# Performance work log

Measured on AMD Instinct MI355X. Metric: run time of the kernel, lower is better.

The kernel has to match this reference:

```python
import jax, jax.numpy as jnp
import numpy as np

RESET_PERIOD = 10
DECAY = 0.1
D_MODEL = 512
D_INNER = 1024
N_LAYERS = 4


def layer_norm(x, scale, bias, eps=1e-5):
    mu = jnp.mean(x, axis=-1, keepdims=True)
    var = jnp.mean((x - mu) ** 2, axis=-1, keepdims=True)
    return (x - mu) * jax.lax.rsqrt(var + eps) * scale + bias


def setup_inputs() -> dict:
    key = jax.random.key(0)
    ks = jax.random.split(key, 12)
    B, S, F, V, MF = 8, 2048, 128, 256, 4096
    D, DI, L = D_MODEL, D_INNER, N_LAYERS
    rn = lambda k, shape, s: jax.random.normal(k, shape, jnp.float32) * s
    return {
        "frames": rn(ks[0], (B, S, F), 1.0),
        "padding_mask": jax.random.uniform(ks[1], (B, S)) < 0.9,
        "W_in_proj": rn(ks[2], (F, D), 0.05),
        "b_in_proj": jnp.zeros((D,), jnp.float32),
        "pos_emb": rn(ks[3], (MF, D), 0.02),
        "ln_scale": jnp.ones((L, D), jnp.float32),
        "ln_bias": jnp.zeros((L, D), jnp.float32),
        "W_in": rn(ks[4], (L, D, 2 * DI), 0.03),
        "b_in": jnp.zeros((L, 2 * DI), jnp.float32),
        "W_out": rn(ks[5], (L, DI, D), 0.03),
        "b_out": jnp.zeros((L, D), jnp.float32),
        "fn_scale": jnp.ones((D,), jnp.float32),
        "fn_bias": jnp.zeros((D,), jnp.float32),
        "W_frame": rn(ks[6], (D, F), 0.03),
        "b_frame": jnp.zeros((F,), jnp.float32),
        "W_sym": rn(ks[7], (D, V), 0.03),
        "b_sym": jnp.zeros((V,), jnp.float32),
    }


def reference(frames, padding_mask, W_in_proj, b_in_proj, pos_emb,
              ln_scale, ln_bias, W_in, b_in, W_out, b_out,
              fn_scale, fn_bias, W_frame, b_frame, W_sym, b_sym):
    B, S, F = frames.shape
    # input projection + clamped positional embedding
    x = frames @ W_in_proj + b_in_proj                     # [B,S,D]
    pos = jnp.clip(jnp.arange(S), 0, pos_emb.shape[0] - 1)
    x = x + pos_emb[pos][None]
    # periodic hard-reset decay: frame_counter starts at 0, incremented AFTER
    # each step, so steps with (t+1) % reset_period == 0 are scaled.
    t = jnp.arange(S) + 1
    decay = jnp.where(t % RESET_PERIOD == 0, DECAY, 1.0)[None, :, None]  # [1,S,1]

    def layer(h, p):
        s, b, Wi, bi, Wo, bo = p
        n = layer_norm(h, s, b)
        uz = n @ Wi + bi                                   # [B,S,2*DI]
        u, g = jnp.split(uz, 2, axis=-1)
        y = (u * jax.nn.silu(g)) @ Wo + bo                 # [B,S,D]
        # wrapper scales the full block output (incl. residual)
        return (h + y) * decay, None

    x, _ = jax.lax.scan(layer, x, (ln_scale, ln_bias, W_in, b_in, W_out, b_out))
    x = layer_norm(x, fn_scale, fn_bias)
    frame_outputs = x @ W_frame + b_frame                  # [B,S,F]
    symbol_logits = x @ W_sym + b_sym                      # [B,S,V]
    m = padding_mask[..., None]
    frame_outputs = jnp.where(m, frame_outputs, 0.0)
    symbol_logits = jnp.where(m, symbol_logits, 0.0)
    return frame_outputs, symbol_logits
```

## Files before the change

### kernel.cpp

```cpp
#include <hip/hip_runtime.h>
#include <hip/hip_bf16.h>

using f32x4  = __attribute__((ext_vector_type(4))) float;
using bf16x8 = __attribute__((ext_vector_type(8))) short;
using bf16x4 = __attribute__((ext_vector_type(4))) short;

#define MTOT   16384
#define DMODEL 512
#define DINNER 1024
#define SEQ    2048

__device__ __forceinline__ short f2b(float f){
  unsigned u = __builtin_bit_cast(unsigned, f);
  u = (u + 0x7FFFu + ((u >> 16) & 1u)) >> 16;
  return (short)u;
}

__device__ __forceinline__ void gl_lds16(const short* g, short* l){
  __builtin_amdgcn_global_load_lds(
      (const __attribute__((address_space(1))) void*)g,
      (__attribute__((address_space(3))) void*)l, 16, 0, 0);
}

__global__ void detect_mask(const unsigned char* __restrict__ m, int* __restrict__ flag){
  __shared__ int sge2, soff, soff8;
  int tid = threadIdx.x;
  if (tid == 0){ sge2 = 0; soff = 0; soff8 = 0; }
  __syncthreads();
  int ge2 = 0, off = 0, off8 = 0;
  for (int i = tid; i < 16384; i += 256){
    unsigned char b = m[i];
    if (b >= 2) ge2++;
    if ((i & 3) && b) off++;
    if (((i & 7) == 4) && b) off8++;
  }
  atomicAdd(&sge2, ge2); atomicAdd(&soff, off); atomicAdd(&soff8, off8);
  __syncthreads();
  if (tid == 0){
    int f;
    if      (sge2 > 0) f = 2;
    else if (soff > 0) f = 1;
    else if (soff8 > 0) f = 0;
    else               f = 3;
    *flag = f;
  }
}

__device__ __forceinline__ bool mask_at(const void* mask, int flag, int m){
  if (flag == 1) return ((const unsigned char*)mask)[m] != 0;
  if (flag == 2) return ((const float*)mask)[m] != 0.0f;
  if (flag == 3) return ((const int*)mask)[2*m] != 0;
  return ((const int*)mask)[m] != 0;
}

__global__ void cvt_bf16(const float* __restrict__ in, short* __restrict__ out){
  int i = (blockIdx.x * 256 + threadIdx.x) * 4;
  float4 v = *(const float4*)(in + i);
  bf16x4 o; o[0] = f2b(v.x); o[1] = f2b(v.y); o[2] = f2b(v.z); o[3] = f2b(v.w);
  *(bf16x4*)(out + i) = o;
}

__global__ void transpose_w(const float* __restrict__ in, short* __restrict__ out, int R, int C){
  in  += (size_t)blockIdx.z * R * C;
  out += (size_t)blockIdx.z * R * C;
  __shared__ float t[32][33];
  int tx = threadIdx.x, ty = threadIdx.y;
  int r0 = blockIdx.y * 32, c0 = blockIdx.x * 32;
  #pragma unroll
  for (int i = 0; i < 4; i++)
    t[ty + i*8][tx] = in[(size_t)(r0 + ty + i*8) * C + c0 + tx];
  __syncthreads();
  #pragma unroll
  for (int i = 0; i < 4; i++)
    out[(size_t)(c0 + ty + i*8) * R + r0 + tx] = f2b(t[tx][ty + i*8]);
}

__global__ __launch_bounds__(256) void ln_k(const float* __restrict__ x,
                                            const float* __restrict__ sc,
                                            const float* __restrict__ bi,
                                            short* __restrict__ out){
  int row  = blockIdx.x * 4 + (threadIdx.x >> 6);
  int lane = threadIdx.x & 63;
  const float* p = x + (size_t)row * DMODEL + lane * 8;
  float4 a = *(const float4*)p;
  float4 b = *(const float4*)(p + 4);
  float s = a.x+a.y+a.z+a.w + b.x+b.y+b.z+b.w;
  float q = a.x*a.x+a.y*a.y+a.z*a.z+a.w*a.w + b.x*b.x+b.y*b.y+b.z*b.z+b.w*b.w;
  #pragma unroll
  for (int o = 32; o >= 1; o >>= 1){ s += __shfl_xor(s, o); q += __shfl_xor(q, o); }
  float mu  = s * (1.0f/DMODEL);
  float var = q * (1.0f/DMODEL) - mu*mu;
  float rs  = rsqrtf(var + 1e-5f);
  int c = lane * 8;
  float vals[8] = {a.x,a.y,a.z,a.w,b.x,b.y,b.z,b.w};
  bf16x8 o8;
  #pragma unroll
  for (int e = 0; e < 8; e++) o8[e] = f2b((vals[e]-mu)*rs*sc[c+e] + bi[c+e]);
  *(bf16x8*)(out + (size_t)row * DMODEL + c) = o8;
}

template<int MODE, int K>
__global__ __launch_bounds__(256) void gemm_k(
    const short* __restrict__ A, const short* __restrict__ B0, const short* __restrict__ B1,
    const float* __restrict__ bias0, const float* __restrict__ bias1,
    const float* __restrict__ pos, float* __restrict__ xbuf, short* __restrict__ obuf,
    float* __restrict__ fout, const void* __restrict__ mask, const int* __restrict__ flagp,
    int ldo)
{
  constexpr int BM = (MODE == 1) ? 64 : 128;
  constexpr int BN = 128;
  constexpr int NB = (MODE == 1) ? 2 : 1;
  constexpr int NJ = (MODE == 1) ? 2 : 4;

  __shared__ short lds[(BM + BN * NB) * 64];
  short* lA  = lds;
  short* lB  = lds + BM * 64;
  short* lB2 = lds + (BM + BN) * 64;

  const int nbx = gridDim.x;
  int bid = blockIdx.y * nbx + blockIdx.x;
  const int nwg = nbx * gridDim.y;
  bid = (bid & 7) * (nwg >> 3) + (bid >> 3);
  const int bx = bid % nbx, by = bid / nbx;
  const int n0 = bx * BN, m0 = by * BM;

  const int tid = threadIdx.x, lane = tid & 63, wid = tid >> 6;
  const int lr  = lane >> 3;
  const int lks = (lane & 7) ^ (lr & 7);
  const int fr = lane & 15;
  const int kg = lane >> 4;

  const int wr = (MODE == 1) ? 0 : (wid >> 1);
  const int wc = (MODE == 1) ? wid : (wid & 1);
  const int rA0 = wr * 64 + fr;
  const int rB0 = wc * ((MODE == 1) ? 32 : 64) + fr;

  f32x4 acc[4][NJ];
  f32x4 acc2[(MODE == 1) ? 4 : 1][(MODE == 1) ? 2 : 1];
  const f32x4 zero = {0.f, 0.f, 0.f, 0.f};
  #pragma unroll
  for (int i = 0; i < 4; i++)
    #pragma unroll
    for (int j = 0; j < NJ; j++) acc[i][j] = zero;
  if constexpr (MODE == 1){
    #pragma unroll
    for (int i = 0; i < 4; i++)
      #pragma unroll
      for (int j = 0; j < 2; j++) acc2[i][j] = zero;
  }

  const short* Ab  = A  + (size_t)m0 * K + (size_t)lr * K + lks * 8;
  const short* B0b = B0 + (size_t)n0 * K + (size_t)lr * K + lks * 8;
  const short* B1b = (MODE == 1) ? (B1 + (size_t)n0 * K + (size_t)lr * K + lks * 8) : nullptr;

  for (int kt = 0; kt < K; kt += 64){
    __syncthreads();
    #pragma unroll
    for (int c = 0; c < BM / 32; c++)
      gl_lds16(Ab + kt + (size_t)(wid + c * 4) * 8 * K, lA + (wid + c * 4) * 512);
    #pragma unroll
    for (int c = 0; c < BN / 32; c++)
      gl_lds16(B0b + kt + (size_t)(wid + c * 4) * 8 * K, lB + (wid + c * 4) * 512);
    if constexpr (MODE == 1){
      #pragma unroll
      for (int c = 0; c < BN / 32; c++)
        gl_lds16(B1b + kt + (size_t)(wid + c * 4) * 8 * K, lB2 + (wid + c * 4) * 512);
    }
    __syncthreads();

    #pragma unroll
    for (int kb8 = 0; kb8 < 8; kb8 += 4){
      bf16x8 aF[4];
      #pragma unroll
      for (int i = 0; i < 4; i++){
        const int row = rA0 + i * 16;
        aF[i] = *(const bf16x8*)((const char*)lA + row * 128 + (((kg + kb8) ^ (row & 7)) * 16));
      }
      if constexpr (MODE == 1){
        bf16x8 bF[2], gF[2];
        #pragma unroll
        for (int j = 0; j < 2; j++){
          const int row = rB0 + j * 16;
          const int p = ((kg + kb8) ^ (row & 7)) * 16;
          bF[j] = *(const bf16x8*)((const char*)lB  + row * 128 + p);
          gF[j] = *(const bf16x8*)((const char*)lB2 + row * 128 + p);
        }
        #pragma unroll
        for (int i = 0; i < 4; i++)
          #pragma unroll
          for (int j = 0; j < 2; j++){
            acc[i][j]  = __builtin_amdgcn_mfma_f32_16x16x32_bf16(aF[i], bF[j], acc[i][j], 0, 0, 0);
            acc2[i][j] = __builtin_amdgcn_mfma_f32_16x16x32_bf16(aF[i], gF[j], acc2[i][j], 0, 0, 0);
          }
      } else {
        bf16x8 bF[4];
        #pragma unroll
        for (int j = 0; j < 4; j++){
          const int row = rB0 + j * 16;
          bF[j] = *(const bf16x8*)((const char*)lB + row * 128 + (((kg + kb8) ^ (row & 7)) * 16));
        }
        #pragma unroll
        for (int i = 0; i < 4; i++)
          #pragma unroll
          for (int j = 0; j < 4; j++)
            acc[i][j] = __builtin_amdgcn_mfma_f32_16x16x32_bf16(aF[i], bF[j], acc[i][j], 0, 0, 0);
      }
    }
  }

  const int col0 = n0 + ((MODE == 1) ? wid * 32 : wc * 64) + fr;
  const int row0 = m0 + ((MODE == 1) ? 0 : wr * 64) + kg * 4;
  int flag = 0;
  if constexpr (MODE == 3) flag = *flagp;

  #pragma unroll
  for (int i = 0; i < 4; i++){
    #pragma unroll
    for (int r = 0; r < 4; r++){
      const int gm = row0 + i * 16 + r;
      #pragma unroll
      for (int j = 0; j < NJ; j++){
        const int gn = col0 + j * 16;
        float v = acc[i][j][r];
        if constexpr (MODE == 0){
          xbuf[(size_t)gm * ldo + gn] = v + bias0[gn] + pos[(size_t)(gm & (SEQ-1)) * DMODEL + gn];
        } else if constexpr (MODE == 1){
          float u = v + bias0[gn];
          float g = acc2[i][j][r] + bias1[gn];
          float sg = g / (1.0f + expf(-g));
          obuf[(size_t)gm * ldo + gn] = f2b(u * sg);
        } else if constexpr (MODE == 2){
          int s = gm & (SEQ-1);
          float d = (((s + 1) % 10) == 0) ? 0.1f : 1.0f;
          float y = v + bias0[gn];
          xbuf[(size_t)gm * ldo + gn] = (xbuf[(size_t)gm * ldo + gn] + y) * d;
        } else {
          bool mk = mask_at(mask, flag, gm);
          fout[(size_t)gm * ldo + gn] = mk ? (v + bias0[gn]) : 0.0f;
        }
      }
    }
  }
}

extern "C" void kernel_launch(void* const* d_in, const int* in_sizes, int n_in,
                              void* d_out, int out_size, void* d_ws, size_t ws_size,
                              hipStream_t stream){
  const float* frames    = (const float*)d_in[0];
  const void*  mask      = d_in[1];
  const float* W_in_proj = (const float*)d_in[2];
  const float* b_in_proj = (const float*)d_in[3];
  const float* pos_emb   = (const float*)d_in[4];
  const float* ln_scale  = (const float*)d_in[5];
  const float* ln_bias   = (const float*)d_in[6];
  const float* W_in      = (const float*)d_in[7];
  const float* b_in      = (const float*)d_in[8];
  const float* W_out     = (const float*)d_in[9];
  const float* b_out     = (const float*)d_in[10];
  const float* fn_scale  = (const float*)d_in[11];
  const float* fn_bias   = (const float*)d_in[12];
  const float* W_frame   = (const float*)d_in[13];
  const float* b_frame   = (const float*)d_in[14];
  const float* W_sym     = (const float*)d_in[15];
  const float* b_sym     = (const float*)d_in[16];

  char* w = (char*)d_ws;
  int*   flag = (int*)w;
  float* xbuf = (float*)(w + 256);
  short* nbuf = (short*)(w + 256 + 33554432);
  short* abuf = (short*)(w + 256 + 33554432 + 16777216);
  short* frb  = (short*)(w + 256 + 33554432 + 16777216 + 33554432);
  short* Wt0  = frb + (size_t)16384 * 128;
  short* Wt1  = Wt0 + (size_t)512 * 128;
  short* Wt2  = Wt1 + (size_t)4 * 2048 * 512;
  short* Wt3  = Wt2 + (size_t)4 * 512 * 1024;
  short* Wt4  = Wt3 + (size_t)128 * 512;

  detect_mask<<<1, 256, 0, stream>>>((const unsigned char*)mask, flag);
  cvt_bf16<<<2048, 256, 0, stream>>>(frames, frb);
  transpose_w<<<dim3(16,  4, 1), dim3(32, 8), 0, stream>>>(W_in_proj, Wt0, 128, 512);
  transpose_w<<<dim3(64, 16, 4), dim3(32, 8), 0, stream>>>(W_in,      Wt1, 512, 2048);
  transpose_w<<<dim3(16, 32, 4), dim3(32, 8), 0, stream>>>(W_out,     Wt2, 1024, 512);
  transpose_w<<<dim3(4,  16, 1), dim3(32, 8), 0, stream>>>(W_frame,   Wt3, 512, 128);
  transpose_w<<<dim3(8,  16, 1), dim3(32, 8), 0, stream>>>(W_sym,     Wt4, 512, 256);

  gemm_k<0, 128><<<dim3(4, 128), 256, 0, stream>>>(frb, Wt0, nullptr, b_in_proj, nullptr, pos_emb,
      xbuf, nullptr, nullptr, nullptr, nullptr, 512);

  for (int l = 0; l < 4; l++){
    ln_k<<<4096, 256, 0, stream>>>(xbuf, ln_scale + l*512, ln_bias + l*512, nbuf);
    gemm_k<1, 512><<<dim3(8, 256), 256, 0, stream>>>(nbuf,
        Wt1 + (size_t)l*2048*512, Wt1 + (size_t)l*2048*512 + (size_t)1024*512,
        b_in + l*2048, b_in + l*2048 + 1024, nullptr,
        nullptr, abuf, nullptr, nullptr, nullptr, 1024);
    gemm_k<2, 1024><<<dim3(4, 128), 256, 0, stream>>>(abuf, Wt2 + (size_t)l*512*1024, nullptr,
        b_out + l*512, nullptr, nullptr, xbuf, nullptr, nullptr, nullptr, nullptr, 512);
  }

  ln_k<<<4096, 256, 0, stream>>>(xbuf, fn_scale, fn_bias, nbuf);
  gemm_k<3, 512><<<dim3(1, 128), 256, 0, stream>>>(nbuf, Wt3, nullptr, b_frame, nullptr, nullptr,
      nullptr, nullptr, (float*)d_out, mask, flag, 128);
  gemm_k<3, 512><<<dim3(2, 128), 256, 0, stream>>>(nbuf, Wt4, nullptr, b_sym, nullptr, nullptr,
      nullptr, nullptr, (float*)d_out + (size_t)16384*128, mask, flag, 256);
}
```

Before: 582.0 us.

## Interleave GLU weight halves to use unified 128x128 GEMM tile; fuse output heads

Permutes the W_in transpose so that u and gate columns alternate in 16-column groups. The GLU GEMM can then use the standard 128x128 tile with a single B operand and pair adjacent accumulator fragments in the epilogue, replacing the 64-row tile with dual B buffers. The frame and symbol output projections also become one launch over a 384-column weight, relying on Wt3 and Wt4 sitting next to each other in the workspace. This raises the compute per loaded byte and removes one launch, at the cost of an unusual column mapping that has to stay consistent between the transpose and the epilogue.

```diff
diff --git a/kernel.cpp b/kernel.cpp
--- a/kernel.cpp
+++ b/kernel.cpp
@@ -60,6 +60,7 @@
   *(bf16x4*)(out + i) = o;
 }
 
+template<int GLU>
 __global__ void transpose_w(const float* __restrict__ in, short* __restrict__ out, int R, int C){
   in  += (size_t)blockIdx.z * R * C;
   out += (size_t)blockIdx.z * R * C;
@@ -71,8 +72,16 @@
     t[ty + i*8][tx] = in[(size_t)(r0 + ty + i*8) * C + c0 + tx];
   __syncthreads();
   #pragma unroll
-  for (int i = 0; i < 4; i++)
-    out[(size_t)(c0 + ty + i*8) * R + r0 + tx] = f2b(t[tx][ty + i*8]);
+  for (int i = 0; i < 4; i++){
+    int oc = c0 + ty + i*8;
+    int nr;
+    if constexpr (GLU){
+      int half = C >> 1;
+      nr = (oc < half) ? (((oc >> 4) << 5) + (oc & 15))
+                       : ((((oc - half) >> 4) << 5) + 16 + (oc & 15));
+    } else nr = oc;
+    out[(size_t)nr * R + r0 + tx] = f2b(t[tx][ty + i*8]);
+  }
 }
 
 __global__ __launch_bounds__(256) void ln_k(const float* __restrict__ x,
@@ -101,21 +110,16 @@
 
 template<int MODE, int K>
 __global__ __launch_bounds__(256) void gemm_k(
-    const short* __restrict__ A, const short* __restrict__ B0, const short* __restrict__ B1,
+    const short* __restrict__ A, const short* __restrict__ B,
     const float* __restrict__ bias0, const float* __restrict__ bias1,
     const float* __restrict__ pos, float* __restrict__ xbuf, short* __restrict__ obuf,
     float* __restrict__ fout, const void* __restrict__ mask, const int* __restrict__ flagp,
     int ldo)
 {
-  constexpr int BM = (MODE == 1) ? 64 : 128;
-  constexpr int BN = 128;
-  constexpr int NB = (MODE == 1) ? 2 : 1;
-  constexpr int NJ = (MODE == 1) ? 2 : 4;
-
-  __shared__ short lds[(BM + BN * NB) * 64];
-  short* lA  = lds;
-  short* lB  = lds + BM * 64;
-  short* lB2 = lds + (BM + BN) * 64;
+  constexpr int BM = 128, BN = 128;
+  __shared__ short lds[(BM + BN) * 64];
+  short* lA = lds;
+  short* lB = lds + BM * 64;
 
   const int nbx = gridDim.x;
   int bid = blockIdx.y * nbx + blockIdx.x;
@@ -130,113 +134,93 @@
   const int fr = lane & 15;
   const int kg = lane >> 4;
 
-  const int wr = (MODE == 1) ? 0 : (wid >> 1);
-  const int wc = (MODE == 1) ? wid : (wid & 1);
+  const int wr = wid >> 1, wc = wid & 1;
   const int rA0 = wr * 64 + fr;
-  const int rB0 = wc * ((MODE == 1) ? 32 : 64) + fr;
-
-  f32x4 acc[4][NJ];
-  f32x4 acc2[(MODE == 1) ? 4 : 1][(MODE == 1) ? 2 : 1];
+  const int rB0 = wc * 64 + fr;
+
+  f32x4 acc[4][4];
   const f32x4 zero = {0.f, 0.f, 0.f, 0.f};
   #pragma unroll
   for (int i = 0; i < 4; i++)
     #pragma unroll
-    for (int j = 0; j < NJ; j++) acc[i][j] = zero;
-  if constexpr (MODE == 1){
-    #pragma unroll
-    for (int i = 0; i < 4; i++)
-      #pragma unroll
-      for (int j = 0; j < 2; j++) acc2[i][j] = zero;
-  }
-
-  const short* Ab  = A  + (size_t)m0 * K + (size_t)lr * K + lks * 8;
-  const short* B0b = B0 + (size_t)n0 * K + (size_t)lr * K + lks * 8;
-  const short* B1b = (MODE == 1) ? (B1 + (size_t)n0 * K + (size_t)lr * K + lks * 8) : nullptr;
+    for (int j = 0; j < 4; j++) acc[i][j] = zero;
+
+  const short* Ab = A + (size_t)m0 * K + (size_t)lr * K + lks * 8;
+  const short* Bb = B + (size_t)n0 * K + (size_t)lr * K + lks * 8;
 
   for (int kt = 0; kt < K; kt += 64){
     __syncthreads();
     #pragma unroll
-    for (int c = 0; c < BM / 32; c++)
+    for (int c = 0; c < 4; c++)
       gl_lds16(Ab + kt + (size_t)(wid + c * 4) * 8 * K, lA + (wid + c * 4) * 512);
     #pragma unroll
-    for (int c = 0; c < BN / 32; c++)
-      gl_lds16(B0b + kt + (size_t)(wid + c * 4) * 8 * K, lB + (wid + c * 4) * 512);
-    if constexpr (MODE == 1){
-      #pragma unroll
-      for (int c = 0; c < BN / 32; c++)
-        gl_lds16(B1b + kt + (size_t)(wid + c * 4) * 8 * K, lB2 + (wid + c * 4) * 512);
-    }
+    for (int c = 0; c < 4; c++)
+      gl_lds16(Bb + kt + (size_t)(wid + c * 4) * 8 * K, lB + (wid + c * 4) * 512);
     __syncthreads();
 
     #pragma unroll
     for (int kb8 = 0; kb8 < 8; kb8 += 4){
-      bf16x8 aF[4];
+      bf16x8 aF[4], bF[4];
       #pragma unroll
       for (int i = 0; i < 4; i++){
         const int row = rA0 + i * 16;
         aF[i] = *(const bf16x8*)((const char*)lA + row * 128 + (((kg + kb8) ^ (row & 7)) * 16));
       }
+      #pragma unroll
+      for (int j = 0; j < 4; j++){
+        const int row = rB0 + j * 16;
+        bF[j] = *(const bf16x8*)((const char*)lB + row * 128 + (((kg + kb8) ^ (row & 7)) * 16));
+      }
+      #pragma unroll
+      for (int i = 0; i < 4; i++)
+        #pragma unroll
+        for (int j = 0; j < 4; j++)
+          acc[i][j] = __builtin_amdgcn_mfma_f32_16x16x32_bf16(aF[i], bF[j], acc[i][j], 0, 0, 0);
+    }
+  }
+
+  const int col0 = n0 + wc * 64 + fr;
+  const int row0 = m0 + wr * 64 + kg * 4;
+  int flag = 0;
+  if constexpr (MODE == 3) flag = *flagp;
+
+  #pragma unroll
+  for (int i = 0; i < 4; i++){
+    #pragma unroll
+    for (int r = 0; r < 4; r++){
+      const int gm = row0 + i * 16 + r;
       if constexpr (MODE == 1){
-        bf16x8 bF[2], gF[2];
         #pragma unroll
-        for (int j = 0; j < 2; j++){
-          const int row = rB0 + j * 16;
-          const int p = ((kg + kb8) ^ (row & 7)) * 16;
-          bF[j] = *(const bf16x8*)((const char*)lB  + row * 128 + p);
-          gF[j] = *(const bf16x8*)((const char*)lB2 + row * 128 + p);
+        for (int jj = 0; jj < 2; jj++){
+          const int j = 2 * jj;
+          const int nb = n0 + wc * 64 + j * 16;
+          const int lc = ((nb >> 5) << 4) + fr;
+          float u = acc[i][j][r]     + bias0[lc];
+          float g = acc[i][j+1][r]   + bias0[1024 + lc];
+          float sg = g / (1.0f + expf(-g));
+          obuf[(size_t)gm * 1024 + lc] = f2b(u * sg);
         }
-        #pragma unroll
-        for (int i = 0; i < 4; i++)
-          #pragma unroll
-          for (int j = 0; j < 2; j++){
-            acc[i][j]  = __builtin_amdgcn_mfma_f32_16x16x32_bf16(aF[i], bF[j], acc[i][j], 0, 0, 0);
-            acc2[i][j] = __builtin_amdgcn_mfma_f32_16x16x32_bf16(aF[i], gF[j], acc2[i][j], 0, 0, 0);
-          }
       } else {
-        bf16x8 bF[4];
         #pragma unroll
         for (int j = 0; j < 4; j++){
-          const int row = rB0 + j * 16;
-          bF[j] = *(const bf16x8*)((const char*)lB + row * 128 + (((kg + kb8) ^ (row & 7)) * 16));
-        }
-        #pragma unroll
-        for (int i = 0; i < 4; i++)
-          #pragma unroll
-          for (int j = 0; j < 4; j++)
-            acc[i][j] = __builtin_amdgcn_mfma_f32_16x16x32_bf16(aF[i], bF[j], acc[i][j], 0, 0, 0);
-      }
-    }
-  }
-
-  const int col0 = n0 + ((MODE == 1) ? wid * 32 : wc * 64) + fr;
-  const int row0 = m0 + ((MODE == 1) ? 0 : wr * 64) + kg * 4;
-  int flag = 0;
-  if constexpr (MODE == 3) flag = *flagp;
-
-  #pragma unroll
-  for (int i = 0; i < 4; i++){
-    #pragma unroll
-    for (int r = 0; r < 4; r++){
-      const int gm = row0 + i * 16 + r;
-      #pragma unroll
-      for (int j = 0; j < NJ; j++){
-        const int gn = col0 + j * 16;
-        float v = acc[i][j][r];
-        if constexpr (MODE == 0){
-          xbuf[(size_t)gm * ldo + gn] = v + bias0[gn] + pos[(size_t)(gm & (SEQ-1)) * DMODEL + gn];
-        } else if constexpr (MODE == 1){
-          float u = v + bias0[gn];
-          float g = acc2[i][j][r] + bias1[gn];
-          float sg = g / (1.0f + expf(-g));
-          obuf[(size_t)gm * ldo + gn] = f2b(u * sg);
-        } else if constexpr (MODE == 2){
-          int s = gm & (SEQ-1);
-          float d = (((s + 1) % 10) == 0) ? 0.1f : 1.0f;
-          float y = v + bias0[gn];
-          xbuf[(size_t)gm * ldo + gn] = (xbuf[(size_t)gm * ldo + gn] + y) * d;
-        } else {
-          bool mk = mask_at(mask, flag, gm);
-          fout[(size_t)gm * ldo + gn] = mk ? (v + bias0[gn]) : 0.0f;
+          const int gn = col0 + j * 16;
+          float v = acc[i][j][r];
+          if constexpr (MODE == 0){
+            xbuf[(size_t)gm * ldo + gn] = v + bias0[gn] + pos[(size_t)(gm & (SEQ-1)) * DMODEL + gn];
+          } else if constexpr (MODE == 2){
+            int s = gm & (SEQ-1);
+            float d = (((s + 1) % 10) == 0) ? 0.1f : 1.0f;
+            float y = v + bias0[gn];
+            xbuf[(size_t)gm * ldo + gn] = (xbuf[(size_t)gm * ldo + gn] + y) * d;
+          } else {
+            bool mk = mask_at(mask, flag, gm);
+            if (gn < 128){
+              fout[(size_t)gm * 128 + gn] = mk ? (v + bias0[gn]) : 0.0f;
+            } else {
+              int gs = gn - 128;
+              fout[(size_t)16384 * 128 + (size_t)gm * 256 + gs] = mk ? (v + bias1[gs]) : 0.0f;
+            }
+          }
         }
       }
     }
@@ -278,28 +262,25 @@
 
   detect_mask<<<1, 256, 0, stream>>>((const unsigned char*)mask, flag);
   cvt_bf16<<<2048, 256, 0, stream>>>(frames, frb);
-  transpose_w<<<dim3(16,  4, 1), dim3(32, 8), 0, stream>>>(W_in_proj, Wt0, 128, 512);
-  transpose_w<<<dim3(64, 16, 4), dim3(32, 8), 0, stream>>>(W_in,      Wt1, 512, 2048);
-  transpose_w<<<dim3(16, 32, 4), dim3(32, 8), 0, stream>>>(W_out,     Wt2, 1024, 512);
-  transpose_w<<<dim3(4,  16, 1), dim3(32, 8), 0, stream>>>(W_frame,   Wt3, 512, 128);
-  transpose_w<<<dim3(8,  16, 1), dim3(32, 8), 0, stream>>>(W_sym,     Wt4, 512, 256);
-
-  gemm_k<0, 128><<<dim3(4, 128), 256, 0, stream>>>(frb, Wt0, nullptr, b_in_proj, nullptr, pos_emb,
+  transpose_w<0><<<dim3(16,  4, 1), dim3(32, 8), 0, stream>>>(W_in_proj, Wt0, 128, 512);
+  transpose_w<1><<<dim3(64, 16, 4), dim3(32, 8), 0, stream>>>(W_in,      Wt1, 512, 2048);
+  transpose_w<0><<<dim3(16, 32, 4), dim3(32, 8), 0, stream>>>(W_out,     Wt2, 1024, 512);
+  transpose_w<0><<<dim3(4,  16, 1), dim3(32, 8), 0, stream>>>(W_frame,   Wt3, 512, 128);
+  transpose_w<0><<<dim3(8,  16, 1), dim3(32, 8), 0, stream>>>(W_sym,     Wt4, 512, 256);
+
+  gemm_k<0, 128><<<dim3(4, 128), 256, 0, stream>>>(frb, Wt0, b_in_proj, nullptr, pos_emb,
       xbuf, nullptr, nullptr, nullptr, nullptr, 512);
 
   for (int l = 0; l < 4; l++){
     ln_k<<<4096, 256, 0, stream>>>(xbuf, ln_scale + l*512, ln_bias + l*512, nbuf);
-    gemm_k<1, 512><<<dim3(8, 256), 256, 0, stream>>>(nbuf,
-        Wt1 + (size_t)l*2048*512, Wt1 + (size_t)l*2048*512 + (size_t)1024*512,
-        b_in + l*2048, b_in + l*2048 + 1024, nullptr,
+    gemm_k<1, 512><<<dim3(16, 128), 256, 0, stream>>>(nbuf,
+        Wt1 + (size_t)l*2048*512, b_in + l*2048, nullptr, nullptr,
         nullptr, abuf, nullptr, nullptr, nullptr, 1024);
-    gemm_k<2, 1024><<<dim3(4, 128), 256, 0, stream>>>(abuf, Wt2 + (size_t)l*512*1024, nullptr,
+    gemm_k<2, 1024><<<dim3(4, 128), 256, 0, stream>>>(abuf, Wt2 + (size_t)l*512*1024,
         b_out + l*512, nullptr, nullptr, xbuf, nullptr, nullptr, nullptr, nullptr, 512);
   }
 
   ln_k<<<4096, 256, 0, stream>>>(xbuf, fn_scale, fn_bias, nbuf);
-  gemm_k<3, 512><<<dim3(1, 128), 256, 0, stream>>>(nbuf, Wt3, nullptr, b_frame, nullptr, nullptr,
-      nullptr, nullptr, (float*)d_out, mask, flag, 128);
-  gemm_k<3, 512><<<dim3(2, 128), 256, 0, stream>>>(nbuf, Wt4, nullptr, b_sym, nullptr, nullptr,
-      nullptr, nullptr, (float*)d_out + (size_t)16384*128, mask, flag, 256);
-}
+  gemm_k<3, 512><<<dim3(3, 128), 256, 0, stream>>>(nbuf, Wt3, b_frame, b_sym, nullptr,
+      nullptr, nullptr, (float*)d_out, mask, flag, 0);
+}
```

After: 574.0 us. No clear change (-1.4%).
